# Optimization experiments

Measured on AMD Instinct MI355X. Metric: run time of the kernel, lower is better.

## Reference

```python
import jax, jax.numpy as jnp
import numpy as np

WIDTH = 8    # hwcfg['width']: bitstream code width, BinGen scale = 2**WIDTH
DEPTH = 12   # hwcfg['depth']: FSUAdd accumulator depth, bound = 2**DEPTH - 1


def setup_inputs() -> dict:
    key = jax.random.key(0)
    k1, k2 = jax.random.split(key)
    batch, in_f, out_f = 4096, 2048, 4096
    # stochastic-computing input: one bit per element for the current cycle
    x = jax.random.bernoulli(k1, 0.5, (batch, in_f)).astype(jnp.float32)
    # bipolar weight probabilities in [-1, 1] (weight_ext)
    w = jax.random.uniform(k2, (out_f, in_f), jnp.float32, -1.0, 1.0)
    # Sobol RNG sample for the current cycle, values live in [0, 2**WIDTH)
    rng_val = jnp.ones((1,), jnp.float32) * 128.0
    return {"input": x, "weight": w, "rng_val": rng_val}


def reference(input, weight, rng_val):
    """One cycle of FSUMatMul: static bipolar FSUMul + scaled bipolar FSUAdd (first cycle, acc=0)."""
    batch, in_f = input.shape
    # ---- FSUMul (static, bipolar) ----
    prob = (weight + 1.0) * 0.5                      # bipolar value -> unipolar probability
    source = jnp.round(prob * (2.0 ** WIDTH))        # BinGen: quantized binary source
    path = (source > rng_val[0]).astype(input.dtype)  # BSGen bit for each weight, (out, in)
    # product bit = XNOR(x, path) = 1 - |x - path| on {0,1} bits.
    # Sum over in_features of the (batch,out,in) broadcast product, computed exactly
    # via the GEMM identity: sum_k 1-|x-p| = in_f - (sum x + sum p - 2 * x @ p^T).
    sx = jnp.sum(input, axis=1)                      # (batch,)
    sp = jnp.sum(path, axis=1)                       # (out,)
    xp = jnp.einsum('bi,oi->bo', input, path)        # (batch, out) GEMM
    sum_prod = in_f - (sx[:, None] + sp[None, :] - 2.0 * xp)
    # ---- FSUAdd (bipolar, scaled: scale_carry = entry = in_f -> offset = 0) ----
    scale_carry = jnp.float32(in_f)
    acc = jnp.clip(sum_prod, 0.0, 2.0 ** DEPTH - 1)  # first-cycle accumulator state (init 0)
    out = (acc >= scale_carry).astype(jnp.float32)   # emitted output bit per (batch, out)
    return out
```

## Files before the change

### kernel.cpp

```cpp
#include <hip/hip_runtime.h>


#define BATCH 4096
#define INF   2048
#define OUTF  4096

typedef unsigned long long u64;
typedef float f4 __attribute__((ext_vector_type(4)));

__global__ __launch_bounds__(256) void pack0_kernel(
    const float* __restrict__ x, const float* __restrict__ w,
    const float* __restrict__ rng,
    u64* __restrict__ xp0, u64* __restrict__ pp0)
{
    const int lane = threadIdx.x & 63;
    const int wav  = threadIdx.x >> 6;
    const int id   = blockIdx.x * 4 + wav;

    if (id < BATCH) {
        const float v = x[(size_t)id * INF + lane];
        const u64 b = __ballot(v != 0.0f);
        if (lane == 0) xp0[id] = b;
    } else {
        const int o = id - BATCH;
        const float v = w[(size_t)o * INF + lane];
        const float s = rintf((v + 1.0f) * 0.5f * 256.0f);
        const u64 b = __ballot(s > rng[0]);
        if (lane == 0) pp0[o] = b;
    }
}

__global__ __launch_bounds__(256) void cmp_kernel(
    const u64* __restrict__ xp0, const u64* __restrict__ pp0,
    const float* __restrict__ x, const float* __restrict__ w,
    const float* __restrict__ rng, float* __restrict__ out)
{
    const int tid = threadIdx.x;
    const int o0  = blockIdx.x * 1024 + tid * 4;
    const int b0  = blockIdx.y * 8;

    const u64 p0 = pp0[o0 + 0];
    const u64 p1 = pp0[o0 + 1];
    const u64 p2 = pp0[o0 + 2];
    const u64 p3 = pp0[o0 + 3];

    #pragma unroll
    for (int i = 0; i < 8; ++i) {
        const int b = b0 + i;
        const u64 xv = xp0[b];
        bool eq0 = (p0 == xv);
        bool eq1 = (p1 == xv);
        bool eq2 = (p2 == xv);
        bool eq3 = (p3 == xv);
        if (eq0 | eq1 | eq2 | eq3) {
            const float r = rng[0];
            bool eq[4] = {eq0, eq1, eq2, eq3};
            for (int j = 0; j < 4; ++j) {
                if (!eq[j]) continue;
                const int o = o0 + j;
                bool all = true;
                for (int k = 64; k < INF; ++k) {
                    const bool xb = x[(size_t)b * INF + k] != 0.0f;
                    const bool pb =
                        rintf((w[(size_t)o * INF + k] + 1.0f) * 0.5f * 256.0f) > r;
                    all = all && (xb == pb);
                }
                eq[j] = all;
            }
            eq0 = eq[0]; eq1 = eq[1]; eq2 = eq[2]; eq3 = eq[3];
        }
        f4 res = { eq0 ? 1.0f : 0.0f, eq1 ? 1.0f : 0.0f,
                   eq2 ? 1.0f : 0.0f, eq3 ? 1.0f : 0.0f };
        *reinterpret_cast<f4*>(out + (size_t)b * OUTF + o0) = res;
    }
}

extern "C" void kernel_launch(void* const* d_in, const int* in_sizes, int n_in,
                              void* d_out, int out_size, void* d_ws, size_t ws_size,
                              hipStream_t stream) {
    const float* x   = (const float*)d_in[0];
    const float* w   = (const float*)d_in[1];
    const float* rng = (const float*)d_in[2];
    float* out = (float*)d_out;

    u64* xp0 = (u64*)d_ws;
    u64* pp0 = xp0 + BATCH;

    pack0_kernel<<<dim3((BATCH + OUTF) / 4), dim3(256), 0, stream>>>(
        x, w, rng, xp0, pp0);

    cmp_kernel<<<dim3(OUTF / 1024, BATCH / 8), dim3(256), 0, stream>>>(
        xp0, pp0, x, w, rng, out);
}
```

Baseline: 107.2 us.

## Zero output with memset and write only matching entries from LDS-staged batch keys

```diff
diff --git a/kernel.cpp b/kernel.cpp
--- a/kernel.cpp
+++ b/kernel.cpp
@@ -6,7 +6,6 @@
 #define OUTF  4096
 
 typedef unsigned long long u64;
-typedef float f4 __attribute__((ext_vector_type(4)));
 
 __global__ __launch_bounds__(256) void pack0_kernel(
     const float* __restrict__ x, const float* __restrict__ w,
@@ -30,48 +29,35 @@
     }
 }
 
-__global__ __launch_bounds__(256) void cmp_kernel(
+__global__ __launch_bounds__(256) void match_kernel(
     const u64* __restrict__ xp0, const u64* __restrict__ pp0,
     const float* __restrict__ x, const float* __restrict__ w,
     const float* __restrict__ rng, float* __restrict__ out)
 {
+    __shared__ u64 xq[64];
+
     const int tid = threadIdx.x;
-    const int o0  = blockIdx.x * 1024 + tid * 4;
-    const int b0  = blockIdx.y * 8;
+    const int o   = blockIdx.x * 256 + tid;
+    const int b0  = blockIdx.y * 64;
 
-    const u64 p0 = pp0[o0 + 0];
-    const u64 p1 = pp0[o0 + 1];
-    const u64 p2 = pp0[o0 + 2];
-    const u64 p3 = pp0[o0 + 3];
+    if (tid < 64) xq[tid] = xp0[b0 + tid];
+    const u64 p = pp0[o];
+    __syncthreads();
 
-    #pragma unroll
-    for (int i = 0; i < 8; ++i) {
-        const int b = b0 + i;
-        const u64 xv = xp0[b];
-        bool eq0 = (p0 == xv);
-        bool eq1 = (p1 == xv);
-        bool eq2 = (p2 == xv);
-        bool eq3 = (p3 == xv);
-        if (eq0 | eq1 | eq2 | eq3) {
+    #pragma unroll 8
+    for (int i = 0; i < 64; ++i) {
+        if (p == xq[i]) {
+            const int b = b0 + i;
             const float r = rng[0];
-            bool eq[4] = {eq0, eq1, eq2, eq3};
-            for (int j = 0; j < 4; ++j) {
-                if (!eq[j]) continue;
-                const int o = o0 + j;
-                bool all = true;
-                for (int k = 64; k < INF; ++k) {
-                    const bool xb = x[(size_t)b * INF + k] != 0.0f;
-                    const bool pb =
-                        rintf((w[(size_t)o * INF + k] + 1.0f) * 0.5f * 256.0f) > r;
-                    all = all && (xb == pb);
-                }
-                eq[j] = all;
+            bool all = true;
+            for (int k = 64; k < INF; ++k) {
+                const bool xb = x[(size_t)b * INF + k] != 0.0f;
+                const bool pb =
+                    rintf((w[(size_t)o * INF + k] + 1.0f) * 0.5f * 256.0f) > r;
+                all = all && (xb == pb);
             }
-            eq0 = eq[0]; eq1 = eq[1]; eq2 = eq[2]; eq3 = eq[3];
+            if (all) out[(size_t)b * OUTF + o] = 1.0f;
         }
-        f4 res = { eq0 ? 1.0f : 0.0f, eq1 ? 1.0f : 0.0f,
-                   eq2 ? 1.0f : 0.0f, eq3 ? 1.0f : 0.0f };
-        *reinterpret_cast<f4*>(out + (size_t)b * OUTF + o0) = res;
     }
 }
 
@@ -86,9 +72,11 @@
     u64* xp0 = (u64*)d_ws;
     u64* pp0 = xp0 + BATCH;
 
+    hipMemsetAsync(out, 0, (size_t)out_size, stream);
+
     pack0_kernel<<<dim3((BATCH + OUTF) / 4), dim3(256), 0, stream>>>(
         x, w, rng, xp0, pp0);
 
-    cmp_kernel<<<dim3(OUTF / 1024, BATCH / 8), dim3(256), 0, stream>>>(
+    match_kernel<<<dim3(OUTF / 256, BATCH / 64), dim3(256), 0, stream>>>(
         xp0, pp0, x, w, rng, out);
 }
```

Result: no change. 106.8 us (-0.3%).
